# Optimization experiments

Measured on AMD Instinct MI355X. Metric: run time of the kernel, lower is better.

The kernel has to match this reference:

```python
import jax, jax.numpy as jnp
import numpy as np

NUM_CLASSES = 33  # labels 0..32; class 0 = background, 32 instances
EPS = 1e-06


def _lovasz_hinge_flat(logits, labels):
    # logits, labels: flat 1-D float arrays (labels in {0,1})
    signs = 2.0 * labels - 1.0
    errors = 1.0 - logits * signs
    order = jnp.argsort(-errors)            # descending sort
    errors_sorted = errors[order]
    gt_sorted = labels[order]
    gts = jnp.sum(gt_sorted)
    intersection = gts - jnp.cumsum(gt_sorted)
    union = gts + jnp.cumsum(1.0 - gt_sorted)
    jaccard = 1.0 - intersection / union
    grad = jnp.concatenate([jaccard[:1], jaccard[1:] - jaccard[:-1]])
    return jnp.dot(jax.nn.relu(errors_sorted), grad)


def _per_sample_loss(y_emb, y_sig, gt_patch):
    # y_emb: [2,H,W] float, y_sig: [1,H,W] float, gt_patch: [1,H,W] int
    # to_onehot(gt)[0, 1:] -> [N,H,W], N = NUM_CLASSES-1 instance channels
    gt_one_hot = jax.nn.one_hot(gt_patch[0], NUM_CLASSES, axis=0, dtype=y_emb.dtype)[1:]
    counts = jnp.sum(gt_one_hot, axis=(1, 2), keepdims=True)          # [N,1,1]
    # per-instance embedding centers: [2,N,1,1]
    centers = jnp.sum(gt_one_hot[None] * y_emb[:, None], axis=(2, 3), keepdims=True) / counts
    instance_sigmas = gt_one_hot[None] * y_sig[:, None]               # [1,N,H,W]
    sigmas = jnp.sum(instance_sigmas, axis=(2, 3), keepdims=True) / counts  # [1,N,1,1]
    var_sigmas = jnp.sum(((instance_sigmas - jax.lax.stop_gradient(sigmas)) * gt_one_hot) ** 2) / counts  # [N,1,1]
    center_dist = jnp.linalg.norm(centers - y_emb[:, None], axis=0)   # [N,H,W]
    probs = jnp.exp(-0.5 * (center_dist / sigmas) ** 2)               # [1,N,H,W]
    logits = (probs * 2.0 - 1.0).reshape(-1)
    labels = jnp.broadcast_to(gt_one_hot[None], probs.shape).reshape(-1)
    return _lovasz_hinge_flat(logits, labels) + jnp.mean(var_sigmas)


def setup_inputs() -> dict:
    key = jax.random.key(0)
    k1, k2, k3 = jax.random.split(key, 3)
    B, H, W = 4, 512, 512
    y_embeddings = jax.random.normal(k1, (B, 2, H, W), dtype=jnp.float32)
    y_sigma = jax.random.uniform(k2, (B, 1, H, W), dtype=jnp.float32)
    y_true = jax.random.randint(k3, (B, 1, H, W), 0, NUM_CLASSES, dtype=jnp.int64)
    return {"y_embeddings": y_embeddings, "y_sigma": y_sigma, "y_true": y_true}


def reference(y_embeddings, y_sigma, y_true):
    # Assumes every sample contains foreground (random labels over 512x512
    # guarantee this w.h.p.), so the torch `if torch.any(gt>0)` branch is taken
    # for all samples and the final loss is the mean over the batch.
    losses = jax.vmap(_per_sample_loss)(y_embeddings, y_sigma, y_true)
    return jnp.mean(losses)
```

## Files before the change

kernel.cpp:

```cpp
#include <hip/hip_runtime.h>

#define HW    262144
#define BNUM  4
#define NC    33
#define NI    32

#define NB     1024
#define BSCALE 64.0f
#define EG     4096
#define ESCALE 2048.0f

typedef unsigned long long ull;

#define W_CNTB 8192
#define W_CNTF 8196
#define W_FINL 8200
#define W_VART 8204
#define W_CONS 8208
#define W_PART 8736
#define PJ 168
#define PS (128 * PJ)

__global__ void __launch_bounds__(256) stats_kernel(
    const float* __restrict__ emb, const float* __restrict__ sig,
    const int* __restrict__ gt, float* __restrict__ ws) {
  int s = blockIdx.y;
  int j = blockIdx.x;
  int t = threadIdx.x;
  int w = t >> 6;
  __shared__ float acc[4][165];
  int bid = s * 128 + j;
  unsigned* wsu = (unsigned*)ws;
  const float* e0p = emb + (size_t)s * 2 * HW;
  const float* e1p = e0p + HW;
  const float* sp  = sig + (size_t)s * HW;
  const int*   gp  = gt  + (size_t)s * HW;
  int idx0 = j * 2048 + t * 4;
  int idx1 = idx0 + 1024;
  int4   lb0 = *(const int4*)(gp + idx0);
  int4   lb1 = *(const int4*)(gp + idx1);
  float4 x0  = *(const float4*)(e0p + idx0);
  float4 x1  = *(const float4*)(e0p + idx1);
  float4 y0  = *(const float4*)(e1p + idx0);
  float4 y1  = *(const float4*)(e1p + idx1);
  float4 sg0 = *(const float4*)(sp + idx0);
  float4 sg1 = *(const float4*)(sp + idx1);
  if (t < 16) {
    wsu[bid * 16 + t] = 0u;
    if (bid == 0) wsu[8192 + t] = 0u;
  }
  for (int k = t; k < 4 * 165; k += 256) ((float*)acc)[k] = 0.f;
  __syncthreads();
#define ACC(L, X, Y, SG)                                                   \
    if (L > 0) {                                                           \
      atomicAdd(&acc[w][L], X);        atomicAdd(&acc[w][33 + L], Y);      \
      atomicAdd(&acc[w][66 + L], SG);  atomicAdd(&acc[w][99 + L], (SG)*(SG)); \
      atomicAdd(&acc[w][132 + L], 1.0f);                                   \
    }
  ACC(lb0.x, x0.x, y0.x, sg0.x)
  ACC(lb0.y, x0.y, y0.y, sg0.y)
  ACC(lb0.z, x0.z, y0.z, sg0.z)
  ACC(lb0.w, x0.w, y0.w, sg0.w)
  ACC(lb1.x, x1.x, y1.x, sg1.x)
  ACC(lb1.y, x1.y, y1.y, sg1.y)
  ACC(lb1.z, x1.z, y1.z, sg1.z)
  ACC(lb1.w, x1.w, y1.w, sg1.w)
#undef ACC
  __syncthreads();
  if (t < 165) {
    float v = acc[0][t] + acc[1][t] + acc[2][t] + acc[3][t];
    ws[W_PART + s * PS + j * PJ + t] = v;
  }
}

__global__ void __launch_bounds__(512) cons_kernel(float* __restrict__ ws) {
  int s = blockIdx.x;
  int t = threadIdx.x;
  int lane = t & 63, wid = t >> 6;
  __shared__ float sums2[2][165];
  __shared__ float sums[165];
  if (t < 330) {
    int r = (t >= 165) ? 1 : 0;
    int c = t - r * 165;
    const float* pp = ws + W_PART + s * PS + (r << 6) * PJ + c;
    float sum = 0.f;
    #pragma unroll 16
    for (int jj = 0; jj < 64; ++jj) sum += pp[jj * PJ];
    sums2[r][c] = sum;
  }
  __syncthreads();
  if (t < 165) sums[t] = sums2[0][t] + sums2[1][t];
  __syncthreads();
  if (t >= 1 && t < NC) {
    float c = sums[132 + t];
    float4 C;
    if (c > 0.f) {
      float inv = 1.0f / c;
      float c0 = sums[t] * inv, c1 = sums[33 + t] * inv, sgm = sums[66 + t] * inv;
      float Q = 0.5f / (sgm * sgm) * BSCALE;
      C.x = Q; C.y = -2.0f * Q * c0; C.z = -2.0f * Q * c1;
      C.w = Q * (c0 * c0 + c1 * c1);
    } else {
      C.x = 0.f; C.y = 0.f; C.z = 0.f; C.w = (float)NB;
    }
    ((float4*)(ws + W_CONS))[s * NC + t] = C;
  }
  if (wid == 0) {
    float S = 0.f, rcp = 0.f;
    if (lane >= 1 && lane < NC) {
      float c = sums[132 + lane];
      if (c > 0.f) {
        float sg = sums[66 + lane] / c;
        S = sums[99 + lane] - c * sg * sg;
        rcp = 1.0f / c;
      }
    }
    for (int o = 32; o; o >>= 1) {
      S   += __shfl_down(S, o);
      rcp += __shfl_down(rcp, o);
    }
    if (lane == 0) ws[W_VART + s] = S * rcp / (float)NI;
  }
}

__global__ void __launch_bounds__(512) hist_scan_kernel(
    const float* __restrict__ emb, const int* __restrict__ gt,
    float* __restrict__ ws, float* __restrict__ out) {
  int s  = blockIdx.y;
  int lb = blockIdx.x;
  __shared__ unsigned hist[NB * 8];
  __shared__ float4 cons[NC];
  __shared__ ull wsum[8];
  __shared__ float red[8];
  __shared__ int flag;
  int t = threadIdx.x;
  int lane = t & 63, wid = t >> 6;
  const float* e0p = emb + (size_t)s * 2 * HW;
  const float* e1p = e0p + HW;
  const int*   gp  = gt  + (size_t)s * HW;
  int base = lb * 4096 + t * 4;
  int4   lbl0 = *(const int4*)(gp + base);
  int4   lbl1 = *(const int4*)(gp + base + 2048);
  float4 px0  = *(const float4*)(e0p + base);
  float4 px1  = *(const float4*)(e0p + base + 2048);
  float4 py0  = *(const float4*)(e1p + base);
  float4 py1  = *(const float4*)(e1p + base + 2048);
  for (int k = t; k < NB * 8; k += 512) hist[k] = 0u;
  if (t < NC) cons[t] = ((const float4*)(ws + W_CONS))[s * NC + t];
  float4 ss0, ss1;
  ss0.x = fmaf(px0.x, px0.x, py0.x * py0.x);
  ss0.y = fmaf(px0.y, px0.y, py0.y * py0.y);
  ss0.z = fmaf(px0.z, px0.z, py0.z * py0.z);
  ss0.w = fmaf(px0.w, px0.w, py0.w * py0.w);
  ss1.x = fmaf(px1.x, px1.x, py1.x * py1.x);
  ss1.y = fmaf(px1.y, px1.y, py1.y * py1.y);
  ss1.z = fmaf(px1.z, px1.z, py1.z * py1.z);
  ss1.w = fmaf(px1.w, px1.w, py1.w * py1.w);
  __syncthreads();
  unsigned* hr = hist + (t & 7);
#define POSFIX(P0, P1, SV, L)                                            \
    if (L > 0) {                                                         \
      float4 C = cons[L];                                                \
      float bf = fmaf(C.x, SV, fmaf(C.y, P0, fmaf(C.z, P1, C.w)));       \
      int ib = min((int)bf, NB - 1);                                     \
      atomicAdd(&hr[ib << 3], 0xFFFFu);                                  \
    }
  POSFIX(px0.x, py0.x, ss0.x, lbl0.x)
  POSFIX(px0.y, py0.y, ss0.y, lbl0.y)
  POSFIX(px0.z, py0.z, ss0.z, lbl0.z)
  POSFIX(px0.w, py0.w, ss0.w, lbl0.w)
  POSFIX(px1.x, py1.x, ss1.x, lbl1.x)
  POSFIX(px1.y, py1.y, ss1.y, lbl1.y)
  POSFIX(px1.z, py1.z, ss1.z, lbl1.z)
  POSFIX(px1.w, py1.w, ss1.w, lbl1.w)
#undef POSFIX
  #pragma unroll 4
  for (int n = 1; n <= NI; ++n) {
    float4 C = cons[n];
#define ITEM(P0, P1, SV)                                               \
    {                                                                  \
      float bf = fmaf(C.x, SV, fmaf(C.y, P0, fmaf(C.z, P1, C.w)));     \
      int ib = min((int)bf, NB - 1);                                   \
      atomicAdd(&hr[ib << 3], 1u);                                     \
    }
    ITEM(px0.x, py0.x, ss0.x)
    ITEM(px0.y, py0.y, ss0.y)
    ITEM(px0.z, py0.z, ss0.z)
    ITEM(px0.w, py0.w, ss0.w)
    ITEM(px1.x, py1.x, ss1.x)
    ITEM(px1.y, py1.y, ss1.y)
    ITEM(px1.z, py1.z, ss1.z)
    ITEM(px1.w, py1.w, ss1.w)
#undef ITEM
  }
  __syncthreads();
  ull* th = ((ull*)ws) + (size_t)s * NB;
  for (int k = t; k < NB; k += 512) {
    uint4 a = *(uint4*)&hist[k * 8];
    uint4 b = *(uint4*)&hist[k * 8 + 4];
    unsigned v = a.x + a.y + a.z + a.w + b.x + b.y + b.z + b.w;
    if (v) {
      ull add = ((ull)(v >> 16) << 32) | (v & 0xFFFFu);
      atomicAdd(&th[k], add);
    }
  }
  __syncthreads();
  if (t == 0) {
    __threadfence();
    flag = (atomicAdd((unsigned*)ws + W_CNTB + s, 1u) == 63u);
  }
  __syncthreads();
  if (!flag) return;

  unsigned* ep = hist;
  unsigned* en = hist + EG;
  for (int k = t; k < 2 * EG; k += 512) hist[k] = 0u;
  float vart = ws[W_VART + s];
  __syncthreads();
  for (int b = t; b < NB; b += 512) {
    ull v = atomicAdd(&th[b], 0ull);
    unsigned pos = (unsigned)(v >> 32), neg = (unsigned)(v & 0xFFFFFFFFu);
    if (pos | neg) {
      float tc = ((float)b + 0.5f) * (1.0f / BSCALE);
      float ex = __expf(-tc);
      if (pos) {
        float e = 2.0f - 2.0f * ex;
        int k = (int)(e * ESCALE); if (k > EG - 1) k = EG - 1;
        atomicAdd(&ep[k], pos);
      }
      if (neg) {
        float e = 2.0f * ex;
        int k = (int)(e * ESCALE); if (k > EG - 1) k = EG - 1;
        atomicAdd(&en[k], neg);
      }
    }
  }
  __syncthreads();
  const int CH = EG / 512;
  int j0 = t * CH;
  unsigned np = 0, nn = 0;
  for (int k = 0; k < CH; ++k) {
    int b = EG - 1 - (j0 + k);
    np += ep[b]; nn += en[b];
  }
  ull v = ((ull)np << 32) | (ull)nn;
  ull inc = v;
  for (int o = 1; o < 64; o <<= 1) {
    ull u = __shfl_up(inc, o);
    if (lane >= o) inc += u;
  }
  if (lane == 63) wsum[wid] = inc;
  __syncthreads();
  ull offset = 0, total = 0;
  for (int i = 0; i < 8; ++i) {
    ull xr = wsum[i];
    if (i < wid) offset += xr;
    total += xr;
  }
  ull excl = offset + inc - v;
  float P = (float)(unsigned)(total >> 32);
  unsigned p = (unsigned)(excl >> 32), f = (unsigned)(excl & 0xFFFFFFFFu);
  float jprev = 1.0f - (P - (float)p) / (P + (float)f);
  float contrib = 0.f;
  for (int k = 0; k < CH; ++k) {
    int b = EG - 1 - (j0 + k);
    unsigned ap_ = ep[b], an_ = en[b];
    if (ap_ | an_) {
      p += ap_; f += an_;
      float j = 1.0f - (P - (float)p) / (P + (float)f);
      float e = ((float)b + 0.5f) * (2.0f / EG);
      contrib += e * (j - jprev);
      jprev = j;
    }
  }
  for (int o = 32; o; o >>= 1) contrib += __shfl_down(contrib, o);
  if (lane == 0) red[wid] = contrib;
  __syncthreads();
  if (t == 0) {
    float tot = 0.f;
    for (int i = 0; i < 8; ++i) tot += red[i];
    float loss = tot + vart;
    float* fin = ws + W_FINL;
    atomicExch(&fin[s], loss);
    __threadfence();
    unsigned old = atomicAdd((unsigned*)ws + W_CNTF, 1u);
    if (old == BNUM - 1) {
      float a = 0.f;
      for (int i = 0; i < BNUM; ++i) a += atomicAdd(&fin[i], 0.0f);
      out[0] = a * (1.0f / BNUM);
    }
  }
}

extern "C" void kernel_launch(void* const* d_in, const int* in_sizes, int n_in,
                              void* d_out, int out_size, void* d_ws, size_t ws_size,
                              hipStream_t stream) {
  const float* emb = (const float*)d_in[0];
  const float* sig = (const float*)d_in[1];
  const int*   gt  = (const int*)d_in[2];
  float* out = (float*)d_out;
  float* ws  = (float*)d_ws;

  dim3 gA(128, BNUM);
  stats_kernel<<<gA, 256, 0, stream>>>(emb, sig, gt, ws);
  cons_kernel<<<BNUM, 512, 0, stream>>>(ws);
  dim3 gB(64, BNUM);
  hist_scan_kernel<<<gB, 512, 0, stream>>>(emb, gt, ws, out);
}
```

Baseline: 113.9 us.

## Fuse stats, constants and histogram kernels into one with in-kernel grid barrier

Merges the three launches (stats, per-sample constants, histogram+scan) into one fused kernel plus a tiny init kernel. Each block keeps its pixel data in registers. The last block per sample reduces the partial sums and publishes the constants through a ready flag, and all blocks spin on that flag before building histograms. This removes a launch, one global re-read of embeddings and labels, and inter-kernel gaps. It relies on all 256 blocks being co-resident for the spin-wait to avoid deadlock.

```diff
diff --git a/kernel.cpp b/kernel.cpp
--- a/kernel.cpp
+++ b/kernel.cpp
@@ -12,131 +12,44 @@
 
 typedef unsigned long long ull;
 
-#define W_CNTB 8192
-#define W_CNTF 8196
-#define W_FINL 8200
-#define W_VART 8204
-#define W_CONS 8208
-#define W_PART 8736
+#define W_CNTA 8192
+#define W_CRDY 8196
+#define W_CNTB 8200
+#define W_CNTF 8204
+#define W_FINL 8208
+#define W_VART 8212
+#define W_CONS 8216
+#define W_PART 8744
 #define PJ 168
-#define PS (128 * PJ)
-
-__global__ void __launch_bounds__(256) stats_kernel(
+#define PS (64 * PJ)
+
+__global__ void __launch_bounds__(64) init_kernel(float* __restrict__ ws) {
+  unsigned* wsu = (unsigned*)ws;
+  int t = threadIdx.x;
+  if (t < 16) wsu[W_CNTA + t] = 0u;
+}
+
+__global__ void __launch_bounds__(512) fused_kernel(
     const float* __restrict__ emb, const float* __restrict__ sig,
-    const int* __restrict__ gt, float* __restrict__ ws) {
-  int s = blockIdx.y;
-  int j = blockIdx.x;
+    const int* __restrict__ gt, float* __restrict__ ws,
+    float* __restrict__ out) {
+  int s  = blockIdx.y;
+  int lb = blockIdx.x;
   int t = threadIdx.x;
-  int w = t >> 6;
-  __shared__ float acc[4][165];
-  int bid = s * 128 + j;
+  int lane = t & 63, wid = t >> 6;
+  __shared__ float acc[8][165];
+  __shared__ unsigned hist[NB * 8];
+  __shared__ float sums2[2][165];
+  __shared__ float sums[165];
+  __shared__ float4 consS[NC];
+  __shared__ ull wsum[8];
+  __shared__ float red[8];
+  __shared__ int isred, flag;
   unsigned* wsu = (unsigned*)ws;
+
   const float* e0p = emb + (size_t)s * 2 * HW;
   const float* e1p = e0p + HW;
   const float* sp  = sig + (size_t)s * HW;
-  const int*   gp  = gt  + (size_t)s * HW;
-  int idx0 = j * 2048 + t * 4;
-  int idx1 = idx0 + 1024;
-  int4   lb0 = *(const int4*)(gp + idx0);
-  int4   lb1 = *(const int4*)(gp + idx1);
-  float4 x0  = *(const float4*)(e0p + idx0);
-  float4 x1  = *(const float4*)(e0p + idx1);
-  float4 y0  = *(const float4*)(e1p + idx0);
-  float4 y1  = *(const float4*)(e1p + idx1);
-  float4 sg0 = *(const float4*)(sp + idx0);
-  float4 sg1 = *(const float4*)(sp + idx1);
-  if (t < 16) {
-    wsu[bid * 16 + t] = 0u;
-    if (bid == 0) wsu[8192 + t] = 0u;
-  }
-  for (int k = t; k < 4 * 165; k += 256) ((float*)acc)[k] = 0.f;
-  __syncthreads();
-#define ACC(L, X, Y, SG)                                                   \
-    if (L > 0) {                                                           \
-      atomicAdd(&acc[w][L], X);        atomicAdd(&acc[w][33 + L], Y);      \
-      atomicAdd(&acc[w][66 + L], SG);  atomicAdd(&acc[w][99 + L], (SG)*(SG)); \
-      atomicAdd(&acc[w][132 + L], 1.0f);                                   \
-    }
-  ACC(lb0.x, x0.x, y0.x, sg0.x)
-  ACC(lb0.y, x0.y, y0.y, sg0.y)
-  ACC(lb0.z, x0.z, y0.z, sg0.z)
-  ACC(lb0.w, x0.w, y0.w, sg0.w)
-  ACC(lb1.x, x1.x, y1.x, sg1.x)
-  ACC(lb1.y, x1.y, y1.y, sg1.y)
-  ACC(lb1.z, x1.z, y1.z, sg1.z)
-  ACC(lb1.w, x1.w, y1.w, sg1.w)
-#undef ACC
-  __syncthreads();
-  if (t < 165) {
-    float v = acc[0][t] + acc[1][t] + acc[2][t] + acc[3][t];
-    ws[W_PART + s * PS + j * PJ + t] = v;
-  }
-}
-
-__global__ void __launch_bounds__(512) cons_kernel(float* __restrict__ ws) {
-  int s = blockIdx.x;
-  int t = threadIdx.x;
-  int lane = t & 63, wid = t >> 6;
-  __shared__ float sums2[2][165];
-  __shared__ float sums[165];
-  if (t < 330) {
-    int r = (t >= 165) ? 1 : 0;
-    int c = t - r * 165;
-    const float* pp = ws + W_PART + s * PS + (r << 6) * PJ + c;
-    float sum = 0.f;
-    #pragma unroll 16
-    for (int jj = 0; jj < 64; ++jj) sum += pp[jj * PJ];
-    sums2[r][c] = sum;
-  }
-  __syncthreads();
-  if (t < 165) sums[t] = sums2[0][t] + sums2[1][t];
-  __syncthreads();
-  if (t >= 1 && t < NC) {
-    float c = sums[132 + t];
-    float4 C;
-    if (c > 0.f) {
-      float inv = 1.0f / c;
-      float c0 = sums[t] * inv, c1 = sums[33 + t] * inv, sgm = sums[66 + t] * inv;
-      float Q = 0.5f / (sgm * sgm) * BSCALE;
-      C.x = Q; C.y = -2.0f * Q * c0; C.z = -2.0f * Q * c1;
-      C.w = Q * (c0 * c0 + c1 * c1);
-    } else {
-      C.x = 0.f; C.y = 0.f; C.z = 0.f; C.w = (float)NB;
-    }
-    ((float4*)(ws + W_CONS))[s * NC + t] = C;
-  }
-  if (wid == 0) {
-    float S = 0.f, rcp = 0.f;
-    if (lane >= 1 && lane < NC) {
-      float c = sums[132 + lane];
-      if (c > 0.f) {
-        float sg = sums[66 + lane] / c;
-        S = sums[99 + lane] - c * sg * sg;
-        rcp = 1.0f / c;
-      }
-    }
-    for (int o = 32; o; o >>= 1) {
-      S   += __shfl_down(S, o);
-      rcp += __shfl_down(rcp, o);
-    }
-    if (lane == 0) ws[W_VART + s] = S * rcp / (float)NI;
-  }
-}
-
-__global__ void __launch_bounds__(512) hist_scan_kernel(
-    const float* __restrict__ emb, const int* __restrict__ gt,
-    float* __restrict__ ws, float* __restrict__ out) {
-  int s  = blockIdx.y;
-  int lb = blockIdx.x;
-  __shared__ unsigned hist[NB * 8];
-  __shared__ float4 cons[NC];
-  __shared__ ull wsum[8];
-  __shared__ float red[8];
-  __shared__ int flag;
-  int t = threadIdx.x;
-  int lane = t & 63, wid = t >> 6;
-  const float* e0p = emb + (size_t)s * 2 * HW;
-  const float* e1p = e0p + HW;
   const int*   gp  = gt  + (size_t)s * HW;
   int base = lb * 4096 + t * 4;
   int4   lbl0 = *(const int4*)(gp + base);
@@ -145,8 +58,96 @@
   float4 px1  = *(const float4*)(e0p + base + 2048);
   float4 py0  = *(const float4*)(e1p + base);
   float4 py1  = *(const float4*)(e1p + base + 2048);
+  float4 sg0  = *(const float4*)(sp + base);
+  float4 sg1  = *(const float4*)(sp + base + 2048);
+  if (t < 32) wsu[(s * 64 + lb) * 32 + t] = 0u;
+  for (int k = t; k < 8 * 165; k += 512) ((float*)acc)[k] = 0.f;
+  __syncthreads();
+  int w = wid;
+#define ACC(L, X, Y, SG)                                                   \
+    if (L > 0) {                                                           \
+      atomicAdd(&acc[w][L], X);        atomicAdd(&acc[w][33 + L], Y);      \
+      atomicAdd(&acc[w][66 + L], SG);  atomicAdd(&acc[w][99 + L], (SG)*(SG)); \
+      atomicAdd(&acc[w][132 + L], 1.0f);                                   \
+    }
+  ACC(lbl0.x, px0.x, py0.x, sg0.x)
+  ACC(lbl0.y, px0.y, py0.y, sg0.y)
+  ACC(lbl0.z, px0.z, py0.z, sg0.z)
+  ACC(lbl0.w, px0.w, py0.w, sg0.w)
+  ACC(lbl1.x, px1.x, py1.x, sg1.x)
+  ACC(lbl1.y, px1.y, py1.y, sg1.y)
+  ACC(lbl1.z, px1.z, py1.z, sg1.z)
+  ACC(lbl1.w, px1.w, py1.w, sg1.w)
+#undef ACC
+  __syncthreads();
+  if (t < 165) {
+    float v = acc[0][t] + acc[1][t] + acc[2][t] + acc[3][t]
+            + acc[4][t] + acc[5][t] + acc[6][t] + acc[7][t];
+    ws[W_PART + s * PS + lb * PJ + t] = v;
+  }
+  __syncthreads();
+  if (t == 0) {
+    __threadfence();
+    isred = (atomicAdd(wsu + W_CNTA + s, 1u) == 63u);
+  }
+  __syncthreads();
   for (int k = t; k < NB * 8; k += 512) hist[k] = 0u;
-  if (t < NC) cons[t] = ((const float4*)(ws + W_CONS))[s * NC + t];
+  if (isred) {
+    __threadfence();
+    if (t < 330) {
+      int r = (t >= 165) ? 1 : 0;
+      int c = t - r * 165;
+      const float* pp = ws + W_PART + s * PS + (r * 32) * PJ + c;
+      float sum = 0.f;
+      #pragma unroll 8
+      for (int jj = 0; jj < 32; ++jj) sum += pp[jj * PJ];
+      sums2[r][c] = sum;
+    }
+    __syncthreads();
+    if (t < 165) sums[t] = sums2[0][t] + sums2[1][t];
+    __syncthreads();
+    if (t >= 1 && t < NC) {
+      float c = sums[132 + t];
+      float4 C;
+      if (c > 0.f) {
+        float inv = 1.0f / c;
+        float c0 = sums[t] * inv, c1 = sums[33 + t] * inv, sgm = sums[66 + t] * inv;
+        float Q = 0.5f / (sgm * sgm) * BSCALE;
+        C.x = Q; C.y = -2.0f * Q * c0; C.z = -2.0f * Q * c1;
+        C.w = Q * (c0 * c0 + c1 * c1);
+      } else {
+        C.x = 0.f; C.y = 0.f; C.z = 0.f; C.w = (float)NB;
+      }
+      ((float4*)(ws + W_CONS))[s * NC + t] = C;
+    }
+    if (wid == 0) {
+      float S = 0.f, rcp = 0.f;
+      if (lane >= 1 && lane < NC) {
+        float c = sums[132 + lane];
+        if (c > 0.f) {
+          float sg = sums[66 + lane] / c;
+          S = sums[99 + lane] - c * sg * sg;
+          rcp = 1.0f / c;
+        }
+      }
+      for (int o = 32; o; o >>= 1) {
+        S   += __shfl_down(S, o);
+        rcp += __shfl_down(rcp, o);
+      }
+      if (lane == 0) ws[W_VART + s] = S * rcp / (float)NI;
+    }
+    __syncthreads();
+    if (t == 0) {
+      __threadfence();
+      atomicExch(wsu + W_CRDY + s, 1u);
+    }
+  }
+  if (t == 0) {
+    while (atomicAdd(wsu + W_CRDY + s, 0u) == 0u) __builtin_amdgcn_s_sleep(2);
+  }
+  __syncthreads();
+  __threadfence();
+  if (t < NC) consS[t] = ((const float4*)(ws + W_CONS))[s * NC + t];
   float4 ss0, ss1;
   ss0.x = fmaf(px0.x, px0.x, py0.x * py0.x);
   ss0.y = fmaf(px0.y, px0.y, py0.y * py0.y);
@@ -160,7 +161,7 @@
   unsigned* hr = hist + (t & 7);
 #define POSFIX(P0, P1, SV, L)                                            \
     if (L > 0) {                                                         \
-      float4 C = cons[L];                                                \
+      float4 C = consS[L];                                               \
       float bf = fmaf(C.x, SV, fmaf(C.y, P0, fmaf(C.z, P1, C.w)));       \
       int ib = min((int)bf, NB - 1);                                     \
       atomicAdd(&hr[ib << 3], 0xFFFFu);                                  \
@@ -176,7 +177,7 @@
 #undef POSFIX
   #pragma unroll 4
   for (int n = 1; n <= NI; ++n) {
-    float4 C = cons[n];
+    float4 C = consS[n];
 #define ITEM(P0, P1, SV)                                               \
     {                                                                  \
       float bf = fmaf(C.x, SV, fmaf(C.y, P0, fmaf(C.z, P1, C.w)));     \
@@ -207,7 +208,7 @@
   __syncthreads();
   if (t == 0) {
     __threadfence();
-    flag = (atomicAdd((unsigned*)ws + W_CNTB + s, 1u) == 63u);
+    flag = (atomicAdd(wsu + W_CNTB + s, 1u) == 63u);
   }
   __syncthreads();
   if (!flag) return;
@@ -283,7 +284,7 @@
     float* fin = ws + W_FINL;
     atomicExch(&fin[s], loss);
     __threadfence();
-    unsigned old = atomicAdd((unsigned*)ws + W_CNTF, 1u);
+    unsigned old = atomicAdd(wsu + W_CNTF, 1u);
     if (old == BNUM - 1) {
       float a = 0.f;
       for (int i = 0; i < BNUM; ++i) a += atomicAdd(&fin[i], 0.0f);
@@ -301,9 +302,7 @@
   float* out = (float*)d_out;
   float* ws  = (float*)d_ws;
 
-  dim3 gA(128, BNUM);
-  stats_kernel<<<gA, 256, 0, stream>>>(emb, sig, gt, ws);
-  cons_kernel<<<BNUM, 512, 0, stream>>>(ws);
-  dim3 gB(64, BNUM);
-  hist_scan_kernel<<<gB, 512, 0, stream>>>(emb, gt, ws, out);
+  init_kernel<<<1, 64, 0, stream>>>(ws);
+  dim3 g(64, BNUM);
+  fused_kernel<<<g, 512, 0, stream>>>(emb, sig, gt, ws, out);
 }
```

After: 147.2 us. 1.29x slower.
